# Kernel optimization log

Hardware: AMD Instinct MI355X
Metric: run time of the kernel (lower is better)

The kernel has to match this reference:

```python
import jax, jax.numpy as jnp
import numpy as np


def _lstm_last(x, wih, whh, bih, bhh):
    """PyTorch-semantics LSTM over x [B, T, I]; returns last hidden state [B, H].
    Gate order in weights: i, f, g, o (PyTorch convention)."""
    B = x.shape[0]
    H = whh.shape[1]
    b = bih + bhh

    def step(carry, xt):
        h, c = carry
        g = xt @ wih.T + h @ whh.T + b  # [B, 4H]
        i, f, gg, o = jnp.split(g, 4, axis=-1)
        c = jax.nn.sigmoid(f) * c + jax.nn.sigmoid(i) * jnp.tanh(gg)
        h = jax.nn.sigmoid(o) * jnp.tanh(c)
        return (h, c), None

    h0 = jnp.zeros((B, H), x.dtype)
    (h, _), _ = jax.lax.scan(step, (h0, h0), jnp.swapaxes(x, 0, 1))
    return h


def setup_inputs() -> dict:
    key = jax.random.key(0)
    ks = jax.random.split(key, 16)
    B, N, T = 512, 32, 50
    s = 0.05
    return {
        "agent_traj": jax.random.normal(ks[0], (B, T, 2), jnp.float32),
        "neighbour_traj": jax.random.normal(ks[1], (B, N, T, 2), jnp.float32),
        "a_wih": jax.random.normal(ks[2], (256, 2), jnp.float32) * s,
        "a_whh": jax.random.normal(ks[3], (256, 64), jnp.float32) * s,
        "a_bih": jax.random.normal(ks[4], (256,), jnp.float32) * s,
        "a_bhh": jax.random.normal(ks[5], (256,), jnp.float32) * s,
        "n_wih": jax.random.normal(ks[6], (256, 2), jnp.float32) * s,
        "n_whh": jax.random.normal(ks[7], (256, 64), jnp.float32) * s,
        "n_bih": jax.random.normal(ks[8], (256,), jnp.float32) * s,
        "n_bhh": jax.random.normal(ks[9], (256,), jnp.float32) * s,
        "d_wih": jax.random.normal(ks[10], (512, 128), jnp.float32) * s,
        "d_whh": jax.random.normal(ks[11], (512, 128), jnp.float32) * s,
        "d_bih": jax.random.normal(ks[12], (512,), jnp.float32) * s,
        "d_bhh": jax.random.normal(ks[13], (512,), jnp.float32) * s,
        "e_w": jax.random.normal(ks[14], (2, 128), jnp.float32) * s,
        "e_b": jax.random.normal(ks[15], (2,), jnp.float32) * s,
    }


def reference(agent_traj, neighbour_traj, a_wih, a_whh, a_bih, a_bhh,
              n_wih, n_whh, n_bih, n_bhh, d_wih, d_whh, d_bih, d_bhh, e_w, e_b):
    B, N, T, _ = neighbour_traj.shape
    # agent encoder: last hidden state [B, 64]
    agent_emb = _lstm_last(agent_traj, a_wih, a_whh, a_bih, a_bhh)
    # neighbour encoder: batch all B*N ragged sequences as one LSTM call, then mean over neighbours
    nh = _lstm_last(neighbour_traj.reshape(B * N, T, 2), n_wih, n_whh, n_bih, n_bhh)
    neigh_emb = nh.reshape(B, N, 64).mean(axis=1)  # [B, 64]

    h0 = jnp.concatenate([agent_emb, neigh_emb], axis=1)  # [B, 128]
    c0 = jnp.zeros_like(h0)
    db = d_bih + d_bhh

    def dec_step(carry, _):
        h, c = carry
        # LSTMCell with input = h itself
        g = h @ d_wih.T + h @ d_whh.T + db  # [B, 512]
        i, f, gg, o = jnp.split(g, 4, axis=-1)
        c = jax.nn.sigmoid(f) * c + jax.nn.sigmoid(i) * jnp.tanh(gg)
        h = jax.nn.sigmoid(o) * jnp.tanh(c)
        pred = h @ e_w.T + e_b  # [B, 2]
        return (h, c), pred

    _, preds = jax.lax.scan(dec_step, (h0, c0), None, length=30)  # [30, B, 2]
    return jnp.swapaxes(preds, 0, 1)  # [B, 30, 2]
```

## Files before the change

### kernel.cpp

```cpp
#include <hip/hip_runtime.h>
#include <hip/hip_bf16.h>


typedef __attribute__((ext_vector_type(8))) short bf16x8;
typedef __attribute__((ext_vector_type(4))) float f32x4;
typedef unsigned int uint;
typedef unsigned short ushort_t;

#define LOG2E  1.4426950408889634f
#define LOG2E2 2.8853900817779268f

__device__ __forceinline__ float rcp_fast(float x) { return __builtin_amdgcn_rcpf(x); }
__device__ __forceinline__ float exp2_fast(float x) { return __builtin_amdgcn_exp2f(x); }
__device__ __forceinline__ float sigf(float x) { return rcp_fast(1.0f + __expf(-x)); }
__device__ __forceinline__ float tanh_fast(float x) {
    x = fminf(fmaxf(x, -15.0f), 15.0f);
    float e = __expf(2.0f * x);
    return (e - 1.0f) * rcp_fast(e + 1.0f);
}
__device__ __forceinline__ ushort_t bf_hi(float f) {
    union { float f; uint u; } v; v.f = f;
    return (ushort_t)(v.u >> 16);
}
__device__ __forceinline__ ushort_t bf_rtn(float f) {
    union { float f; uint u; } v; v.f = f;
    return (ushort_t)((v.u + 0x7FFFu + ((v.u >> 16) & 1u)) >> 16);
}
__device__ __forceinline__ float bf_f(ushort_t h) {
    union { float f; uint u; } v; v.u = ((uint)h) << 16;
    return v.f;
}

__device__ __forceinline__ float cell_update_p(float xi, float xf, float xg,
                                               float xo, float& c) {
    float pi = exp2_fast(-xi);
    float pf = exp2_fast(-xf);
    float po = exp2_fast(-xo);
    float pg = exp2_fast(fminf(xg, 120.0f));
    float A = 1.0f + pf;
    float B = 1.0f + pi;
    float C = 1.0f + pg;
    float BC = B * C;
    float R  = rcp_fast(A * BC);
    float num = __builtin_fmaf(c, BC, (C - 2.0f) * A);
    float cc = num * R;
    c = cc;
    float e2 = exp2_fast(fminf(cc * LOG2E2, 120.0f));
    return (e2 - 1.0f) * rcp_fast((1.0f + po) * (e2 + 1.0f));
}

#define HS 36

__global__ __launch_bounds__(256, 4) void enc19_kernel(
    const float* __restrict__ ax, const float* __restrict__ nx,
    const float* __restrict__ a_wih, const float* __restrict__ a_whh,
    const float* __restrict__ a_bih, const float* __restrict__ a_bhh,
    const float* __restrict__ n_wih, const float* __restrict__ n_whh,
    const float* __restrict__ n_bih, const float* __restrict__ n_bhh,
    float* __restrict__ nh_out, float* __restrict__ ah_out)
{
    const int tid = threadIdx.x, blk = blockIdx.x;
    const bool agent = (blk >= 1024);
    const int seq0 = (agent ? (blk - 1024) : blk) * 16;
    const float* __restrict__ x   = agent ? ax : nx;
    const float* __restrict__ wih = agent ? a_wih : n_wih;
    const float* __restrict__ whh = agent ? a_whh : n_whh;
    const float* __restrict__ bih = agent ? a_bih : n_bih;
    const float* __restrict__ bhh = agent ? a_bhh : n_bhh;
    float* __restrict__ hout = agent ? ah_out : nh_out;

    const int lane = tid & 63, wv = tid >> 6;
    const int col = lane & 15, quad = lane >> 4;

    __shared__ __attribute__((aligned(16))) uint hb[2][16][HS];
    __shared__ __attribute__((aligned(16))) ushort_t xb[50][16][8];

    bf16x8 Aw[4][2];
    #pragma unroll
    for (int g = 0; g < 4; ++g) {
        const float sc = (g == 2) ? LOG2E2 : LOG2E;
        #pragma unroll
        for (int kt = 0; kt < 2; ++kt) {
            const float* p = whh + (size_t)(g * 64 + 16 * wv + col) * 64 + kt * 32 + quad * 8;
            float4 v0 = *(const float4*)p;
            float4 v1 = *(const float4*)(p + 4);
            float vv[8] = { v0.x, v0.y, v0.z, v0.w, v1.x, v1.y, v1.z, v1.w };
            bf16x8 h8;
            #pragma unroll
            for (int j = 0; j < 8; ++j) h8[j] = (short)bf_rtn(vv[j] * sc);
            Aw[g][kt] = h8;
        }
    }

    bf16x8 Ax[4];
    #pragma unroll
    for (int g = 0; g < 4; ++g) {
        const float sc = (g == 2) ? LOG2E2 : LOG2E;
        bf16x8 a;
        #pragma unroll
        for (int j = 0; j < 8; ++j) a[j] = 0;
        if (quad == 0) {
            const int row = g * 64 + 16 * wv + col;
            float w0 = wih[2 * row] * sc, w1 = wih[2 * row + 1] * sc;
            float b  = (bih[row] + bhh[row]) * sc;
            ushort_t w0h = bf_hi(w0), w1h = bf_hi(w1);
            ushort_t bh  = bf_hi(b);
            a[0] = (short)w0h;
            a[1] = (short)w1h;
            a[2] = (short)bf_hi(w0 - bf_f(w0h));
            a[3] = (short)bf_hi(w1 - bf_f(w1h));
            a[4] = (short)w0h;
            a[5] = (short)w1h;
            a[6] = (short)bh;
            a[7] = (short)bf_hi(b - bf_f(bh));
        }
        Ax[g] = a;
    }

    for (int idx = tid; idx < 50 * 16; idx += 256) {
        const int t = idx >> 4, s = idx & 15;
        const float* xp = x + (size_t)(seq0 + s) * 100 + 2 * t;
        float x0 = xp[0], x1 = xp[1];
        ushort_t h0 = bf_hi(x0), h1 = bf_hi(x1);
        ushort_t* e = &xb[t][s][0];
        e[0] = h0; e[1] = h1;
        e[2] = h0; e[3] = h1;
        e[4] = bf_hi(x0 - bf_f(h0));
        e[5] = bf_hi(x1 - bf_f(h1));
        e[6] = 0x3F80; e[7] = 0x3F80;
    }
    for (int i = tid; i < 16 * HS; i += 256) (&hb[0][0][0])[i] = 0u;
    __syncthreads();

    float c[4] = {0.f, 0.f, 0.f, 0.f};
    float hv[4];
    bf16x8 Bx = *(const bf16x8*)&xb[0][col][0];

    for (int t = 0; t < 50; ++t) {
        const int cur = t & 1, nxt = cur ^ 1;

        const f32x4 z4 = {0.f, 0.f, 0.f, 0.f};
        f32x4 acc[4];
        #pragma unroll
        for (int g = 0; g < 4; ++g)
            acc[g] = __builtin_amdgcn_mfma_f32_16x16x32_bf16(Ax[g], Bx, z4, 0, 0, 0);

        #pragma unroll
        for (int kt = 0; kt < 2; ++kt) {
            bf16x8 Bhi = *(const bf16x8*)&hb[cur][col][kt * 16 + quad * 4];
            #pragma unroll
            for (int g = 0; g < 4; ++g)
                acc[g] = __builtin_amdgcn_mfma_f32_16x16x32_bf16(Aw[g][kt], Bhi, acc[g], 0, 0, 0);
        }

        #pragma unroll
        for (int r = 0; r < 4; ++r)
            hv[r] = cell_update_p(acc[0][r], acc[1][r], acc[2][r], acc[3][r], c[r]);

        {
            __hip_bfloat162 p01 = __float22bfloat162_rn(make_float2(hv[0], hv[1]));
            __hip_bfloat162 p23 = __float22bfloat162_rn(make_float2(hv[2], hv[3]));
            uint2 hi2;
            union { __hip_bfloat162 b; uint u; } c0, c1;
            c0.b = p01; c1.b = p23;
            hi2.x = c0.u;
            hi2.y = c1.u;
            const int di = 8 * wv + 2 * quad;
            *(uint2*)&hb[nxt][col][di] = hi2;
        }
        if (t < 49) Bx = *(const bf16x8*)&xb[t + 1][col][0];
        __syncthreads();
    }

    {
        float4 o4 = make_float4(hv[0], hv[1], hv[2], hv[3]);
        *(float4*)(hout + (size_t)(seq0 + col) * 64 + 16 * wv + 4 * quad) = o4;
    }
}

__global__ __launch_bounds__(512) void dec19_kernel(
    const float* __restrict__ ah, const float* __restrict__ nh,
    const float* __restrict__ d_wih, const float* __restrict__ d_whh,
    const float* __restrict__ d_bih, const float* __restrict__ d_bhh,
    const float* __restrict__ e_w, const float* __restrict__ e_b,
    float* __restrict__ out)
{
    const int tid = threadIdx.x;
    const int blk = blockIdx.x;

    const int u  = tid >> 2;
    const int tt = tid & 3;
    const int r  = tt * 128 + u;

    float w[128];
    #pragma unroll
    for (int k = 0; k < 128; k += 4) {
        float4 aa = *(const float4*)(d_wih + r * 128 + k);
        float4 bb = *(const float4*)(d_whh + r * 128 + k);
        w[k]   = aa.x + bb.x;
        w[k+1] = aa.y + bb.y;
        w[k+2] = aa.z + bb.z;
        w[k+3] = aa.w + bb.w;
    }
    const float bias = d_bih[r] + d_bhh[r];

    __shared__ float hs[2][128];
    __shared__ float cs[2][128];
    __shared__ float gs[2][512];
    __shared__ float ews[2][128];
    __shared__ float ebs[2];

    if (tid < 256) {
        const int s = tid >> 7, j = tid & 127;
        const int gseq = blk * 2 + s;
        float v;
        if (j < 64) {
            v = ah[(size_t)gseq * 64 + j];
        } else {
            float acc = 0.0f;
            for (int n = 0; n < 32; ++n)
                acc += nh[(size_t)(gseq * 32 + n) * 64 + (j - 64)];
            v = acc * (1.0f / 32.0f);
        }
        hs[s][j] = v;
        cs[s][j] = 0.0f;
        ews[s][j] = e_w[tid];
    }
    if (tid < 2) ebs[tid] = e_b[tid];
    __syncthreads();

    for (int t = 0; t < 30; ++t) {
        #pragma unroll
        for (int s = 0; s < 2; ++s) {
            const float4* hp = (const float4*)(&hs[s][0]);
            float a0 = 0.f, a1 = 0.f, a2 = 0.f, a3 = 0.f;
            #pragma unroll
            for (int k = 0; k < 32; ++k) {
                float4 h4 = hp[k];
                a0 = __builtin_fmaf(w[4*k+0], h4.x, a0);
                a1 = __builtin_fmaf(w[4*k+1], h4.y, a1);
                a2 = __builtin_fmaf(w[4*k+2], h4.z, a2);
                a3 = __builtin_fmaf(w[4*k+3], h4.w, a3);
            }
            gs[s][tid] = bias + ((a0 + a1) + (a2 + a3));
        }
        __syncthreads();
        if (tid < 256) {
            const int s = tid >> 7, j = tid & 127;
            float4 g4 = *(const float4*)(&gs[s][4 * j]);
            float ig = sigf(g4.x), fg = sigf(g4.y);
            float gg = tanh_fast(g4.z), og = sigf(g4.w);
            float cc = fg * cs[s][j] + ig * gg;
            cs[s][j] = cc;
            hs[s][j] = og * tanh_fast(cc);
        }
        __syncthreads();
        {
            const int wv = tid >> 6, l = tid & 63;
            if (wv < 4) {
                const int s = wv >> 1, o = wv & 1;
                float p = hs[s][l] * ews[o][l] + hs[s][64 + l] * ews[o][64 + l];
                #pragma unroll
                for (int off = 32; off > 0; off >>= 1) p += __shfl_down(p, off);
                if (l == 0) out[((size_t)(blk * 2 + s) * 30 + t) * 2 + o] = p + ebs[o];
            }
        }
    }
}

extern "C" void kernel_launch(void* const* d_in, const int* in_sizes, int n_in,
                              void* d_out, int out_size, void* d_ws, size_t ws_size,
                              hipStream_t stream)
{
    const float* agent_traj = (const float*)d_in[0];
    const float* neigh_traj = (const float*)d_in[1];
    const float* a_wih = (const float*)d_in[2];
    const float* a_whh = (const float*)d_in[3];
    const float* a_bih = (const float*)d_in[4];
    const float* a_bhh = (const float*)d_in[5];
    const float* n_wih = (const float*)d_in[6];
    const float* n_whh = (const float*)d_in[7];
    const float* n_bih = (const float*)d_in[8];
    const float* n_bhh = (const float*)d_in[9];
    const float* d_wih = (const float*)d_in[10];
    const float* d_whh = (const float*)d_in[11];
    const float* d_bih = (const float*)d_in[12];
    const float* d_bhh = (const float*)d_in[13];
    const float* e_w   = (const float*)d_in[14];
    const float* e_b   = (const float*)d_in[15];
    float* out = (float*)d_out;

    float* nh_ws = (float*)d_ws;
    float* ah_ws = nh_ws + 16384 * 64;

    enc19_kernel<<<dim3(1024 + 32), dim3(256), 0, stream>>>(
        agent_traj, neigh_traj,
        a_wih, a_whh, a_bih, a_bhh,
        n_wih, n_whh, n_bih, n_bhh,
        nh_ws, ah_ws);

    dec19_kernel<<<dim3(256), dim3(512), 0, stream>>>(
        ah_ws, nh_ws, d_wih, d_whh, d_bih, d_bhh, e_w, e_b, out);
}
```

Measured before the change: 246.6 us.

## Rewrite decoder LSTM with bf16 MFMA over 16-sequence tiles

The decoder now processes 16 sequences per block with the summed recurrent weights held as bf16 MFMA fragments in registers, replacing the per-thread fp32 FMA matvec over 2 sequences. Gate activations are fused into a register-resident exp2-based cell update with pre-scaled weights, which removes the gate shared-memory round trip and one barrier per step. Projection output is computed by a single wave from an fp32 copy of h. This cuts the decoder grid from 256 to 32 blocks and adds bf16 rounding error in the recurrence.

```diff
diff --git a/kernel.cpp b/kernel.cpp
--- a/kernel.cpp
+++ b/kernel.cpp
@@ -12,12 +12,6 @@
 
 __device__ __forceinline__ float rcp_fast(float x) { return __builtin_amdgcn_rcpf(x); }
 __device__ __forceinline__ float exp2_fast(float x) { return __builtin_amdgcn_exp2f(x); }
-__device__ __forceinline__ float sigf(float x) { return rcp_fast(1.0f + __expf(-x)); }
-__device__ __forceinline__ float tanh_fast(float x) {
-    x = fminf(fmaxf(x, -15.0f), 15.0f);
-    float e = __expf(2.0f * x);
-    return (e - 1.0f) * rcp_fast(e + 1.0f);
-}
 __device__ __forceinline__ ushort_t bf_hi(float f) {
     union { float f; uint u; } v; v.f = f;
     return (ushort_t)(v.u >> 16);
@@ -51,7 +45,7 @@
 
 #define HS 36
 
-__global__ __launch_bounds__(256, 4) void enc19_kernel(
+__global__ __launch_bounds__(256, 4) void enc21_kernel(
     const float* __restrict__ ax, const float* __restrict__ nx,
     const float* __restrict__ a_wih, const float* __restrict__ a_whh,
     const float* __restrict__ a_bih, const float* __restrict__ a_bhh,
@@ -178,93 +172,133 @@
     }
 }
 
-__global__ __launch_bounds__(512) void dec19_kernel(
+#define DHS 68
+#define FHS 136
+
+__global__ __launch_bounds__(512) void dec21_kernel(
     const float* __restrict__ ah, const float* __restrict__ nh,
     const float* __restrict__ d_wih, const float* __restrict__ d_whh,
     const float* __restrict__ d_bih, const float* __restrict__ d_bhh,
     const float* __restrict__ e_w, const float* __restrict__ e_b,
     float* __restrict__ out)
 {
-    const int tid = threadIdx.x;
-    const int blk = blockIdx.x;
-
-    const int u  = tid >> 2;
-    const int tt = tid & 3;
-    const int r  = tt * 128 + u;
-
-    float w[128];
-    #pragma unroll
-    for (int k = 0; k < 128; k += 4) {
-        float4 aa = *(const float4*)(d_wih + r * 128 + k);
-        float4 bb = *(const float4*)(d_whh + r * 128 + k);
-        w[k]   = aa.x + bb.x;
-        w[k+1] = aa.y + bb.y;
-        w[k+2] = aa.z + bb.z;
-        w[k+3] = aa.w + bb.w;
-    }
-    const float bias = d_bih[r] + d_bhh[r];
-
-    __shared__ float hs[2][128];
-    __shared__ float cs[2][128];
-    __shared__ float gs[2][512];
+    const int tid = threadIdx.x, blk = blockIdx.x;
+    const int lane = tid & 63, wv = tid >> 6;
+    const int col = lane & 15, quad = lane >> 4;
+    const int seqg0 = blk * 16;
+
+    __shared__ __attribute__((aligned(16))) uint  hb2[2][16][DHS];
+    __shared__ __attribute__((aligned(16))) float hsf[2][16][FHS];
     __shared__ float ews[2][128];
     __shared__ float ebs[2];
 
-    if (tid < 256) {
-        const int s = tid >> 7, j = tid & 127;
-        const int gseq = blk * 2 + s;
+    bf16x8 Aw[4][4];
+    #pragma unroll
+    for (int g = 0; g < 4; ++g) {
+        const float sc = (g == 2) ? LOG2E2 : LOG2E;
+        const size_t rowb = (size_t)(g * 128 + 16 * wv + col) * 128;
+        #pragma unroll
+        for (int kt = 0; kt < 4; ++kt) {
+            const float* pa = d_wih + rowb + kt * 32 + quad * 8;
+            const float* pb = d_whh + rowb + kt * 32 + quad * 8;
+            float4 a0 = *(const float4*)pa, a1 = *(const float4*)(pa + 4);
+            float4 b0 = *(const float4*)pb, b1 = *(const float4*)(pb + 4);
+            float vv[8] = { a0.x + b0.x, a0.y + b0.y, a0.z + b0.z, a0.w + b0.w,
+                            a1.x + b1.x, a1.y + b1.y, a1.z + b1.z, a1.w + b1.w };
+            bf16x8 h8;
+            #pragma unroll
+            for (int j = 0; j < 8; ++j) h8[j] = (short)bf_rtn(vv[j] * sc);
+            Aw[g][kt] = h8;
+        }
+    }
+    float bias_[4][4];
+    #pragma unroll
+    for (int g = 0; g < 4; ++g) {
+        const float sc = (g == 2) ? LOG2E2 : LOG2E;
+        #pragma unroll
+        for (int r = 0; r < 4; ++r) {
+            const int row = g * 128 + 16 * wv + 4 * quad + r;
+            bias_[g][r] = (d_bih[row] + d_bhh[row]) * sc;
+        }
+    }
+
+    for (int idx = tid; idx < 16 * 128; idx += 512) {
+        const int seq = idx >> 7, j = idx & 127;
+        const int gseq = seqg0 + seq;
         float v;
         if (j < 64) {
             v = ah[(size_t)gseq * 64 + j];
         } else {
-            float acc = 0.0f;
+            float acc = 0.f;
             for (int n = 0; n < 32; ++n)
                 acc += nh[(size_t)(gseq * 32 + n) * 64 + (j - 64)];
             v = acc * (1.0f / 32.0f);
         }
-        hs[s][j] = v;
-        cs[s][j] = 0.0f;
-        ews[s][j] = e_w[tid];
-    }
+        hsf[0][seq][j] = v;
+        ((ushort_t*)&hb2[0][seq][0])[j] = bf_rtn(v);
+    }
+    if (tid < 256) ews[tid >> 7][tid & 127] = e_w[tid];
     if (tid < 2) ebs[tid] = e_b[tid];
     __syncthreads();
 
+    float c[4] = {0.f, 0.f, 0.f, 0.f};
+    int cur = 0;
     for (int t = 0; t < 30; ++t) {
-        #pragma unroll
-        for (int s = 0; s < 2; ++s) {
-            const float4* hp = (const float4*)(&hs[s][0]);
+        const int nxt = cur ^ 1;
+
+        bf16x8 Bh0 = *(const bf16x8*)&hb2[cur][col][0 * 16 + quad * 4];
+        bf16x8 Bh1 = *(const bf16x8*)&hb2[cur][col][1 * 16 + quad * 4];
+        bf16x8 Bh2 = *(const bf16x8*)&hb2[cur][col][2 * 16 + quad * 4];
+        bf16x8 Bh3 = *(const bf16x8*)&hb2[cur][col][3 * 16 + quad * 4];
+
+        const f32x4 z4 = {0.f, 0.f, 0.f, 0.f};
+        f32x4 acc[4];
+        #pragma unroll
+        for (int g = 0; g < 4; ++g) {
+            f32x4 a = __builtin_amdgcn_mfma_f32_16x16x32_bf16(Aw[g][0], Bh0, z4, 0, 0, 0);
+            a = __builtin_amdgcn_mfma_f32_16x16x32_bf16(Aw[g][1], Bh1, a, 0, 0, 0);
+            a = __builtin_amdgcn_mfma_f32_16x16x32_bf16(Aw[g][2], Bh2, a, 0, 0, 0);
+            a = __builtin_amdgcn_mfma_f32_16x16x32_bf16(Aw[g][3], Bh3, a, 0, 0, 0);
+            acc[g] = a;
+        }
+
+        float hv[4];
+        #pragma unroll
+        for (int r = 0; r < 4; ++r)
+            hv[r] = cell_update_p(acc[0][r] + bias_[0][r], acc[1][r] + bias_[1][r],
+                                  acc[2][r] + bias_[2][r], acc[3][r] + bias_[3][r], c[r]);
+
+        {
+            union { __hip_bfloat162 b; uint u; } q0, q1;
+            q0.b = __float22bfloat162_rn(make_float2(hv[0], hv[1]));
+            q1.b = __float22bfloat162_rn(make_float2(hv[2], hv[3]));
+            uint2 hi2; hi2.x = q0.u; hi2.y = q1.u;
+            *(uint2*)&hb2[nxt][col][8 * wv + 2 * quad] = hi2;
+            *(float4*)&hsf[nxt][col][16 * wv + 4 * quad] =
+                make_float4(hv[0], hv[1], hv[2], hv[3]);
+        }
+        __syncthreads();
+
+        if (wv == 7) {
+            const int pr = lane >> 1, half = lane & 1;
+            const int seq = pr >> 1, o = pr & 1;
+            const float4* hp = (const float4*)&hsf[nxt][seq][half * 64];
+            const float4* wp = (const float4*)&ews[o][half * 64];
             float a0 = 0.f, a1 = 0.f, a2 = 0.f, a3 = 0.f;
             #pragma unroll
-            for (int k = 0; k < 32; ++k) {
-                float4 h4 = hp[k];
-                a0 = __builtin_fmaf(w[4*k+0], h4.x, a0);
-                a1 = __builtin_fmaf(w[4*k+1], h4.y, a1);
-                a2 = __builtin_fmaf(w[4*k+2], h4.z, a2);
-                a3 = __builtin_fmaf(w[4*k+3], h4.w, a3);
+            for (int k = 0; k < 16; ++k) {
+                float4 h4 = hp[k], w4 = wp[k];
+                a0 = __builtin_fmaf(h4.x, w4.x, a0);
+                a1 = __builtin_fmaf(h4.y, w4.y, a1);
+                a2 = __builtin_fmaf(h4.z, w4.z, a2);
+                a3 = __builtin_fmaf(h4.w, w4.w, a3);
             }
-            gs[s][tid] = bias + ((a0 + a1) + (a2 + a3));
-        }
-        __syncthreads();
-        if (tid < 256) {
-            const int s = tid >> 7, j = tid & 127;
-            float4 g4 = *(const float4*)(&gs[s][4 * j]);
-            float ig = sigf(g4.x), fg = sigf(g4.y);
-            float gg = tanh_fast(g4.z), og = sigf(g4.w);
-            float cc = fg * cs[s][j] + ig * gg;
-            cs[s][j] = cc;
-            hs[s][j] = og * tanh_fast(cc);
-        }
-        __syncthreads();
-        {
-            const int wv = tid >> 6, l = tid & 63;
-            if (wv < 4) {
-                const int s = wv >> 1, o = wv & 1;
-                float p = hs[s][l] * ews[o][l] + hs[s][64 + l] * ews[o][64 + l];
-                #pragma unroll
-                for (int off = 32; off > 0; off >>= 1) p += __shfl_down(p, off);
-                if (l == 0) out[((size_t)(blk * 2 + s) * 30 + t) * 2 + o] = p + ebs[o];
-            }
-        }
+            float p = (a0 + a1) + (a2 + a3);
+            p += __shfl_xor(p, 1);
+            if (half == 0)
+                out[((size_t)(seqg0 + seq) * 30 + t) * 2 + o] = p + ebs[o];
+        }
+        cur = nxt;
     }
 }
 
@@ -293,12 +327,12 @@
     float* nh_ws = (float*)d_ws;
     float* ah_ws = nh_ws + 16384 * 64;
 
-    enc19_kernel<<<dim3(1024 + 32), dim3(256), 0, stream>>>(
+    enc21_kernel<<<dim3(1024 + 32), dim3(256), 0, stream>>>(
         agent_traj, neigh_traj,
         a_wih, a_whh, a_bih, a_bhh,
         n_wih, n_whh, n_bih, n_bhh,
         nh_ws, ah_ws);
 
-    dec19_kernel<<<dim3(256), dim3(512), 0, stream>>>(
+    dec21_kernel<<<dim3(32), dim3(512), 0, stream>>>(
         ah_ws, nh_ws, d_wih, d_whh, d_bih, d_bhh, e_w, e_b, out);
 }
```

Measured after the change: 257.8 us. 4.6% more time.

## Pack decoder weights as bf16 and run one sequence per block

Applied to the files above, without the earlier changes.

The decoder now keeps its combined recurrent weights in registers as packed bf16 pairs, halving weight register use. This lets launch bounds request 4 waves per SIMD, and the grid doubles to 512 blocks with one sequence each instead of two. The neighbour-mean initialisation is split across four threads per column with a partial-sum reduction. The cost is bf16 rounding of the decoder weights and extra shift/mask ops per FMA.

```diff
diff --git a/kernel.cpp b/kernel.cpp
--- a/kernel.cpp
+++ b/kernel.cpp
@@ -29,6 +29,9 @@
 __device__ __forceinline__ float bf_f(ushort_t h) {
     union { float f; uint u; } v; v.u = ((uint)h) << 16;
     return v.f;
+}
+__device__ __forceinline__ float u_as_f(uint u) {
+    union { float f; uint u; } v; v.u = u; return v.f;
 }
 
 __device__ __forceinline__ float cell_update_p(float xi, float xf, float xg,
@@ -51,7 +54,7 @@
 
 #define HS 36
 
-__global__ __launch_bounds__(256, 4) void enc19_kernel(
+__global__ __launch_bounds__(256, 4) void enc22_kernel(
     const float* __restrict__ ax, const float* __restrict__ nx,
     const float* __restrict__ a_wih, const float* __restrict__ a_whh,
     const float* __restrict__ a_bih, const float* __restrict__ a_bhh,
@@ -178,7 +181,7 @@
     }
 }
 
-__global__ __launch_bounds__(512) void dec19_kernel(
+__global__ __launch_bounds__(512, 4) void dec22_kernel(
     const float* __restrict__ ah, const float* __restrict__ nh,
     const float* __restrict__ d_wih, const float* __restrict__ d_whh,
     const float* __restrict__ d_bih, const float* __restrict__ d_bhh,
@@ -186,83 +189,86 @@
     float* __restrict__ out)
 {
     const int tid = threadIdx.x;
-    const int blk = blockIdx.x;
+    const int seq = blockIdx.x;
 
     const int u  = tid >> 2;
     const int tt = tid & 3;
     const int r  = tt * 128 + u;
 
-    float w[128];
+    uint wp[64];
     #pragma unroll
     for (int k = 0; k < 128; k += 4) {
         float4 aa = *(const float4*)(d_wih + r * 128 + k);
         float4 bb = *(const float4*)(d_whh + r * 128 + k);
-        w[k]   = aa.x + bb.x;
-        w[k+1] = aa.y + bb.y;
-        w[k+2] = aa.z + bb.z;
-        w[k+3] = aa.w + bb.w;
+        union { __hip_bfloat162 b; uint u; } p0, p1;
+        p0.b = __float22bfloat162_rn(make_float2(aa.x + bb.x, aa.y + bb.y));
+        p1.b = __float22bfloat162_rn(make_float2(aa.z + bb.z, aa.w + bb.w));
+        wp[k / 2]     = p0.u;
+        wp[k / 2 + 1] = p1.u;
     }
     const float bias = d_bih[r] + d_bhh[r];
 
-    __shared__ float hs[2][128];
-    __shared__ float cs[2][128];
-    __shared__ float gs[2][512];
+    __shared__ float hs[128];
+    __shared__ float cs[128];
+    __shared__ float gs[512];
     __shared__ float ews[2][128];
     __shared__ float ebs[2];
+    __shared__ float pmean[64][4];
 
     if (tid < 256) {
-        const int s = tid >> 7, j = tid & 127;
-        const int gseq = blk * 2 + s;
-        float v;
-        if (j < 64) {
-            v = ah[(size_t)gseq * 64 + j];
-        } else {
-            float acc = 0.0f;
-            for (int n = 0; n < 32; ++n)
-                acc += nh[(size_t)(gseq * 32 + n) * 64 + (j - 64)];
-            v = acc * (1.0f / 32.0f);
-        }
-        hs[s][j] = v;
-        cs[s][j] = 0.0f;
-        ews[s][j] = e_w[tid];
-    }
+        const int j = tid >> 2, m = tid & 3;
+        float acc = 0.0f;
+        for (int n = m * 8; n < m * 8 + 8; ++n)
+            acc += nh[(size_t)(seq * 32 + n) * 64 + j];
+        pmean[j][m] = acc;
+    }
+    if (tid < 64) {
+        hs[tid] = ah[(size_t)seq * 64 + tid];
+        cs[tid] = 0.0f;
+        cs[64 + tid] = 0.0f;
+    }
+    if (tid < 256) ews[tid >> 7][tid & 127] = e_w[tid];
     if (tid < 2) ebs[tid] = e_b[tid];
     __syncthreads();
+    if (tid < 64)
+        hs[64 + tid] = (pmean[tid][0] + pmean[tid][1] + pmean[tid][2] + pmean[tid][3])
+                       * (1.0f / 32.0f);
+    __syncthreads();
 
     for (int t = 0; t < 30; ++t) {
-        #pragma unroll
-        for (int s = 0; s < 2; ++s) {
-            const float4* hp = (const float4*)(&hs[s][0]);
+        {
+            const float4* hp = (const float4*)(&hs[0]);
             float a0 = 0.f, a1 = 0.f, a2 = 0.f, a3 = 0.f;
             #pragma unroll
             for (int k = 0; k < 32; ++k) {
                 float4 h4 = hp[k];
-                a0 = __builtin_fmaf(w[4*k+0], h4.x, a0);
-                a1 = __builtin_fmaf(w[4*k+1], h4.y, a1);
-                a2 = __builtin_fmaf(w[4*k+2], h4.z, a2);
-                a3 = __builtin_fmaf(w[4*k+3], h4.w, a3);
+                uint u0 = wp[2 * k], u1 = wp[2 * k + 1];
+                a0 = __builtin_fmaf(u_as_f(u0 << 16),          h4.x, a0);
+                a1 = __builtin_fmaf(u_as_f(u0 & 0xFFFF0000u),  h4.y, a1);
+                a2 = __builtin_fmaf(u_as_f(u1 << 16),          h4.z, a2);
+                a3 = __builtin_fmaf(u_as_f(u1 & 0xFFFF0000u),  h4.w, a3);
             }
-            gs[s][tid] = bias + ((a0 + a1) + (a2 + a3));
+            gs[tid] = bias + ((a0 + a1) + (a2 + a3));
         }
         __syncthreads();
-        if (tid < 256) {
-            const int s = tid >> 7, j = tid & 127;
-            float4 g4 = *(const float4*)(&gs[s][4 * j]);
+        if (tid < 128) {
+            const int j = tid;
+            float4 g4 = *(const float4*)(&gs[4 * j]);
             float ig = sigf(g4.x), fg = sigf(g4.y);
             float gg = tanh_fast(g4.z), og = sigf(g4.w);
-            float cc = fg * cs[s][j] + ig * gg;
-            cs[s][j] = cc;
-            hs[s][j] = og * tanh_fast(cc);
+            float cc = fg * cs[j] + ig * gg;
+            cs[j] = cc;
+            hs[j] = og * tanh_fast(cc);
         }
         __syncthreads();
         {
             const int wv = tid >> 6, l = tid & 63;
-            if (wv < 4) {
-                const int s = wv >> 1, o = wv & 1;
-                float p = hs[s][l] * ews[o][l] + hs[s][64 + l] * ews[o][64 + l];
+            if (wv < 2) {
+                const int o = wv;
+                float p = hs[l] * ews[o][l] + hs[64 + l] * ews[o][64 + l];
                 #pragma unroll
                 for (int off = 32; off > 0; off >>= 1) p += __shfl_down(p, off);
-                if (l == 0) out[((size_t)(blk * 2 + s) * 30 + t) * 2 + o] = p + ebs[o];
+                if (l == 0) out[((size_t)seq * 30 + t) * 2 + o] = p + ebs[o];
             }
         }
     }
@@ -293,12 +299,12 @@
     float* nh_ws = (float*)d_ws;
     float* ah_ws = nh_ws + 16384 * 64;
 
-    enc19_kernel<<<dim3(1024 + 32), dim3(256), 0, stream>>>(
+    enc22_kernel<<<dim3(1024 + 32), dim3(256), 0, stream>>>(
         agent_traj, neigh_traj,
         a_wih, a_whh, a_bih, a_bhh,
         n_wih, n_whh, n_bih, n_bhh,
         nh_ws, ah_ws);
 
-    dec19_kernel<<<dim3(256), dim3(512), 0, stream>>>(
+    dec22_kernel<<<dim3(512), dim3(512), 0, stream>>>(
         ah_ws, nh_ws, d_wih, d_whh, d_bih, d_bhh, e_w, e_b, out);
 }
```

Result: slower. 660.2 us (+167.7%).
